# Kernel tuning notes

Measured on AMD Instinct MI355X. Metric: run time of the kernel, lower is better.

The kernel has to match this reference:

```python
import jax, jax.numpy as jnp
import numpy as np

HIDDEN = 256
HORIZON = 24
FMET = 16
OUT = 1
EPS = 1e-5


def setup_inputs() -> dict:
    key = jax.random.key(0)
    ks = jax.random.split(key, 12)
    B, N = 16, 1000
    final_h = jax.random.normal(ks[0], (B, N, HIDDEN), dtype=jnp.float32)
    future_met = jax.random.normal(ks[1], (B, HORIZON, N, FMET), dtype=jnp.float32)
    # step_queries: xavier_uniform over (max_horizon, hidden)
    lim_q = float(np.sqrt(6.0 / (HORIZON + HIDDEN)))
    step_queries = jax.random.uniform(ks[2], (HORIZON, HIDDEN), minval=-lim_q, maxval=lim_q, dtype=jnp.float32)
    # future_met_proj: Linear(FMET -> HIDDEN); store weight as (FMET, HIDDEN)
    lim_fm = float(np.sqrt(1.0 / FMET))
    W_fm = jax.random.uniform(ks[3], (FMET, HIDDEN), minval=-lim_fm, maxval=lim_fm, dtype=jnp.float32)
    b_fm = jax.random.uniform(ks[4], (HIDDEN,), minval=-lim_fm, maxval=lim_fm, dtype=jnp.float32)
    gamma = jnp.ones((HIDDEN,), dtype=jnp.float32)
    beta = jnp.zeros((HIDDEN,), dtype=jnp.float32)
    lim1 = float(np.sqrt(1.0 / HIDDEN))
    W1 = jax.random.uniform(ks[5], (HIDDEN, HIDDEN), minval=-lim1, maxval=lim1, dtype=jnp.float32)
    b1 = jax.random.uniform(ks[6], (HIDDEN,), minval=-lim1, maxval=lim1, dtype=jnp.float32)
    W2 = jax.random.uniform(ks[7], (HIDDEN, OUT), minval=-lim1, maxval=lim1, dtype=jnp.float32)
    b2 = jax.random.uniform(ks[8], (OUT,), minval=-lim1, maxval=lim1, dtype=jnp.float32)
    return {
        "final_h": final_h,
        "future_met": future_met,
        "step_queries": step_queries,
        "W_fm": W_fm,
        "b_fm": b_fm,
        "gamma": gamma,
        "beta": beta,
        "W1": W1,
        "b1": b1,
        "W2": W2,
        "b2": b2,
    }


def _layer_norm(x, gamma, beta):
    mu = jnp.mean(x, axis=-1, keepdims=True)
    var = jnp.mean(jnp.square(x - mu), axis=-1, keepdims=True)
    return (x - mu) * jax.lax.rsqrt(var + EPS) * gamma + beta


def reference(final_h, future_met, step_queries, W_fm, b_fm, gamma, beta, W1, b1, W2, b2):
    # final_h: (B, N, H); future_met: (B, T, N, F)
    # combined: (B, N, T, H) = broadcast(final_h) + queries + proj(future_met)
    combined = final_h[:, :, None, :] + step_queries[None, None, :, :]
    fm = jnp.transpose(future_met, (0, 2, 1, 3))  # (B, N, T, F)
    combined = combined + (jnp.einsum("bntf,fh->bnth", fm, W_fm) + b_fm)
    x = _layer_norm(combined, gamma, beta)
    x = jax.nn.gelu(x @ W1 + b1, approximate=False)
    # dropout is identity in eval mode
    out = x @ W2 + b2  # (B, N, T, OUT)
    return jnp.transpose(out, (0, 2, 1, 3))  # (B, T, N, OUT)
```

## Files before the change

kernel.cpp:

```cpp
#include <hip/hip_runtime.h>
#include <hip/hip_bf16.h>
#include <stdint.h>

#define MROWS 32
#define LDA   264
#define FMS   40

typedef __bf16 bf16x8 __attribute__((ext_vector_type(8)));
typedef float  f32x4  __attribute__((ext_vector_type(4)));

__device__ __forceinline__ unsigned short f2bf(float f) {
    union { float f; uint32_t u; } v; v.f = f;
    return (unsigned short)((v.u + 0x7FFFu + ((v.u >> 16) & 1u)) >> 16);
}

__device__ __forceinline__ ushort2 pk_bf16(float a, float b) {
    union { __hip_bfloat162 v; ushort2 u; } c;
    c.v = __float22bfloat162_rn(make_float2(a, b));
    return c.u;
}

__device__ __forceinline__ float gelu_fast(float v) {
    const float t = v * v;
    const float p = fmaf(0.044715f, t, 1.0f);
    const float u = v * p;
    const float e = __builtin_amdgcn_exp2f(u * -2.3021131160186336f);
    return v * __builtin_amdgcn_rcpf(1.0f + e);
}

__global__ __launch_bounds__(256) void prep1(const float* __restrict__ W1,
                                             const float* __restrict__ step_q,
                                             const float* __restrict__ b_fm,
                                             const float* __restrict__ W_fm,
                                             const float* __restrict__ gamma,
                                             const float* __restrict__ beta,
                                             unsigned short* __restrict__ w1frag,
                                             float* __restrict__ sqb,
                                             unsigned short* __restrict__ wfmfrag,
                                             float* __restrict__ gpart,
                                             float* __restrict__ bpart) {
    const int blk = blockIdx.x, tid = threadIdx.x;
    if (blk < 8) {
        __shared__ unsigned short T[256][40];
        const int kk = blk;
        float sg = 0.f, sb = 0.f;
        #pragma unroll
        for (int r = 0; r < 32; ++r) {
            const int k = (kk << 5) + r;
            const float wv = W1[k * 256 + tid];
            sg = fmaf(gamma[k], wv, sg);
            sb = fmaf(beta[k],  wv, sb);
            T[tid][r] = f2bf(wv);
        }
        gpart[(kk << 8) + tid] = sg;
        bpart[(kk << 8) + tid] = sb;
        __syncthreads();
        #pragma unroll
        for (int f = 0; f < 4; ++f) {
            const int fi = (f << 8) + tid;
            const int l = fi & 63, j = (fi >> 6) & 3, w = fi >> 8;
            const int n = (w << 6) + (j << 4) + (l & 15);
            const uint4 v = *(const uint4*)&T[n][(l >> 4) << 3];
            *(uint4*)&w1frag[((w << 5) + (j << 3) + kk) * 512 + (l << 3)] = v;
        }
    } else if (blk < 32) {
        const int t = blk - 8;
        sqb[t * 256 + tid] = step_q[t * 256 + tid] + b_fm[tid];
    } else {
        const int f  = blk - 32;
        const int fr = (f << 8) + tid;
        const int l = fr & 63, j = (fr >> 6) & 3, w = fr >> 8;
        const int n = (w << 6) + (j << 4) + (l & 15);
        const int qr = l >> 4;
        #pragma unroll
        for (int e = 0; e < 8; ++e) {
            const int k = (qr << 3) + e;
            wfmfrag[(fr << 3) + e] = (k < 16) ? f2bf(W_fm[(k << 8) + n]) : (unsigned short)0;
        }
    }
}

__global__ __launch_bounds__(256) void prep2(const float* __restrict__ gpart,
                                             const float* __restrict__ bpart,
                                             const float* __restrict__ b1,
                                             float* __restrict__ gw1,
                                             float* __restrict__ b1t) {
    const int tid = threadIdx.x;
    float sg = 0.f, sb = 0.f;
    #pragma unroll
    for (int kk = 0; kk < 8; ++kk) {
        sg += gpart[(kk << 8) + tid];
        sb += bpart[(kk << 8) + tid];
    }
    gw1[tid] = sg;
    b1t[tid] = sb + b1[tid];
}

__global__ __launch_bounds__(256, 6) void fused_head(
    const float* __restrict__ final_h, const float* __restrict__ future_met,
    const float* __restrict__ gamma,   const float* __restrict__ W2,
    const float* __restrict__ b2,      const unsigned short* __restrict__ w1frag,
    const float* __restrict__ sqb,     const unsigned short* __restrict__ wfmfrag,
    const float* __restrict__ gw1,     const float* __restrict__ b1t,
    float* __restrict__ out)
{
    __shared__ __align__(16) unsigned short Abuf[MROWS * LDA];
    __shared__ __align__(16) unsigned short fmA[MROWS * FMS];
    __shared__ float2 red[4][MROWS];
    __shared__ float2 mv[MROWS];
    __shared__ float  part[4][MROWS];

    const int tid = threadIdx.x;
    const int w   = tid >> 6;
    const int l   = tid & 63;
    const int col = l & 15;
    const int qr  = l >> 4;
    const int m0  = blockIdx.x * MROWS;
    const int bn0 = m0 / 24;
    const int tt0 = m0 - bn0 * 24;

    if (tid < 128) {
        const int row = tid >> 2, f0 = (tid & 3) << 2;
        const int tta = tt0 + row;
        const int sub = (tta >= 24) + (tta >= 48);
        const int tt  = tta - sub * 24;
        const int bn  = bn0 + sub;
        const int b   = bn / 1000, n = bn - b * 1000;
        const float4 v = *(const float4*)&future_met[((((b * 24 + tt) * 1000) + n) << 4) + f0];
        ushort2 lo = pk_bf16(v.x, v.y), hi = pk_bf16(v.z, v.w);
        ushort4 o; o.x = lo.x; o.y = lo.y; o.z = hi.x; o.w = hi.y;
        *(ushort4*)&fmA[row * FMS + f0] = o;
    }
    {
        const int row = tid >> 3, k = 16 + ((tid & 7) << 1);
        *(unsigned int*)&fmA[row * FMS + k] = 0u;
    }
    __syncthreads();

    float g_[4];
    #pragma unroll
    for (int j = 0; j < 4; ++j) g_[j] = gamma[(w << 6) + (j << 4) + col];

    f32x4 acc[2][4];
    #pragma unroll
    for (int i = 0; i < 2; ++i) {
        #pragma unroll
        for (int r = 0; r < 4; ++r) {
            const int d   = (i << 4) + (qr << 2) + r;
            const int tta = tt0 + d;
            const int sub = (tta >= 24) + (tta >= 48);
            const int tt  = tta - sub * 24;
            const int bn  = bn0 + sub;
            const float* fh = final_h + (bn << 8) + (w << 6) + col;
            const float* sb = sqb + (tt << 8) + (w << 6) + col;
            #pragma unroll
            for (int j = 0; j < 4; ++j)
                acc[i][j][r] = fh[j << 4] + sb[j << 4];
        }
    }
    {
        const bf16x8 af0 = *(const bf16x8*)&fmA[col * FMS + (qr << 3)];
        const bf16x8 af1 = *(const bf16x8*)&fmA[(16 + col) * FMS + (qr << 3)];
        const unsigned short* Bwf = wfmfrag + (w << 11) + (l << 3);
        #pragma unroll
        for (int j = 0; j < 4; ++j) {
            const bf16x8 bf = *(const bf16x8*)(Bwf + (j << 9));
            acc[0][j] = __builtin_amdgcn_mfma_f32_16x16x32_bf16(af0, bf, acc[0][j], 0, 0, 0);
            acc[1][j] = __builtin_amdgcn_mfma_f32_16x16x32_bf16(af1, bf, acc[1][j], 0, 0, 0);
        }
    }

    #pragma unroll
    for (int i = 0; i < 2; ++i) {
        #pragma unroll
        for (int r = 0; r < 4; ++r) {
            const int m = (i << 4) + (qr << 2) + r;
            float s = 0.f, q = 0.f, vj[4];
            #pragma unroll
            for (int j = 0; j < 4; ++j) {
                const float v = acc[i][j][r];
                s += v; q = fmaf(v, v, q);
                vj[j] = v * g_[j];
            }
            s += __shfl_xor(s, 1); q += __shfl_xor(q, 1);
            s += __shfl_xor(s, 2); q += __shfl_xor(q, 2);
            s += __shfl_xor(s, 4); q += __shfl_xor(q, 4);
            s += __shfl_xor(s, 8); q += __shfl_xor(q, 8);
            if (col == 0) red[w][m] = make_float2(s, q);
            const ushort2 p01 = pk_bf16(vj[0], vj[1]);
            const ushort2 p23 = pk_bf16(vj[2], vj[3]);
            unsigned short* Ab = &Abuf[m * LDA + (w << 6) + col];
            Ab[0]  = p01.x; Ab[16] = p01.y;
            Ab[32] = p23.x; Ab[48] = p23.y;
        }
    }
    __syncthreads();

    if (tid < MROWS) {
        const float2 a0 = red[0][tid], a1 = red[1][tid], a2 = red[2][tid], a3 = red[3][tid];
        const float S = a0.x + a1.x + a2.x + a3.x;
        const float Q = a0.y + a1.y + a2.y + a3.y;
        const float mu = S * 0.00390625f;
        const float rstd = rsqrtf(Q * 0.00390625f - mu * mu + 1e-5f);
        mv[tid] = make_float2(mu, rstd);
    }

    #pragma unroll
    for (int i = 0; i < 2; ++i)
        #pragma unroll
        for (int j = 0; j < 4; ++j)
            acc[i][j] = (f32x4){0.f, 0.f, 0.f, 0.f};

    {
        const unsigned short* Bw  = w1frag + (w << 14) + (l << 3);
        const unsigned short* Ab0 = &Abuf[col * LDA + (qr << 3)];
        const unsigned short* Ab1 = &Abuf[(16 + col) * LDA + (qr << 3)];
        #pragma unroll
        for (int kk = 0; kk < 8; ++kk) {
            const bf16x8 a0 = *(const bf16x8*)(Ab0 + (kk << 5));
            const bf16x8 a1 = *(const bf16x8*)(Ab1 + (kk << 5));
            #pragma unroll
            for (int j = 0; j < 4; ++j) {
                const bf16x8 bf = *(const bf16x8*)(Bw + (j << 12) + (kk << 9));
                acc[0][j] = __builtin_amdgcn_mfma_f32_16x16x32_bf16(a0, bf, acc[0][j], 0, 0, 0);
                acc[1][j] = __builtin_amdgcn_mfma_f32_16x16x32_bf16(a1, bf, acc[1][j], 0, 0, 0);
            }
        }
    }

    float gwv[4], btv[4], w2v[4];
    #pragma unroll
    for (int j = 0; j < 4; ++j) {
        const int n = (w << 6) + (j << 4) + col;
        gwv[j] = gw1[n]; btv[j] = b1t[n]; w2v[j] = W2[n];
    }
    __syncthreads();

    #pragma unroll
    for (int i = 0; i < 2; ++i) {
        #pragma unroll
        for (int r = 0; r < 4; ++r) {
            const int m = (i << 4) + (qr << 2) + r;
            const float2 p = mv[m];
            const float cm = -p.x * p.y;
            float pp = 0.f;
            #pragma unroll
            for (int j = 0; j < 4; ++j) {
                const float yv = fmaf(p.y, acc[i][j][r], fmaf(cm, gwv[j], btv[j]));
                const float g = gelu_fast(yv);
                pp = fmaf(g, w2v[j], pp);
            }
            pp += __shfl_xor(pp, 1);
            pp += __shfl_xor(pp, 2);
            pp += __shfl_xor(pp, 4);
            pp += __shfl_xor(pp, 8);
            if (col == 0) part[w][m] = pp;
        }
    }
    __syncthreads();

    if (tid < MROWS) {
        const int m = m0 + tid;
        const float val = part[0][tid] + part[1][tid] + part[2][tid] + part[3][tid] + b2[0];
        const int bn = m / 24, tt = m - bn * 24;
        const int b  = bn / 1000, n = bn - b * 1000;
        out[(b * 24 + tt) * 1000 + n] = val;
    }
}

extern "C" void kernel_launch(void* const* d_in, const int* in_sizes, int n_in,
                              void* d_out, int out_size, void* d_ws, size_t ws_size,
                              hipStream_t stream) {
    const float* final_h    = (const float*)d_in[0];
    const float* future_met = (const float*)d_in[1];
    const float* step_q     = (const float*)d_in[2];
    const float* W_fm       = (const float*)d_in[3];
    const float* b_fm       = (const float*)d_in[4];
    const float* gamma      = (const float*)d_in[5];
    const float* beta       = (const float*)d_in[6];
    const float* W1         = (const float*)d_in[7];
    const float* b1         = (const float*)d_in[8];
    const float* W2         = (const float*)d_in[9];
    const float* b2         = (const float*)d_in[10];

    unsigned short* w1frag  = (unsigned short*)d_ws;
    float*          sqb     = (float*)((char*)d_ws + 131072);
    unsigned short* wfmfrag = (unsigned short*)((char*)d_ws + 155648);
    float*          gw1     = (float*)((char*)d_ws + 188416);
    float*          b1t     = (float*)((char*)d_ws + 189440);
    float*          gpart   = (float*)((char*)d_ws + 190464);
    float*          bpart   = (float*)((char*)d_ws + 198656);
    float* out = (float*)d_out;

    prep1<<<36, 256, 0, stream>>>(W1, step_q, b_fm, W_fm, gamma, beta,
                                  w1frag, sqb, wfmfrag, gpart, bpart);
    prep2<<<1, 256, 0, stream>>>(gpart, bpart, b1, gw1, b1t);
    fused_head<<<12000, 256, 0, stream>>>(final_h, future_met, gamma, W2, b2,
                                          w1frag, sqb, wfmfrag, gw1, b1t, out);
}
```

Baseline: 219.3 us.

## Process two full nodes (48 rows) per block and fold prep2 into main kernel

Each block now handles 48 rows, exactly two (b,n) nodes of 24 horizon steps, instead of 32. This aligns tiles to node boundaries, removes the div/mod index math, and amortizes each W1 fragment load over three MFMA row tiles instead of two. The separate prep2 launch is removed: every block sums the gpart/bpart partials itself, which saves one kernel launch but adds redundant global reads per block. Launch bounds drop from 6 to 5 waves to make room for the larger accumulators and LDS.

```diff
diff --git a/kernel.cpp b/kernel.cpp
--- a/kernel.cpp
+++ b/kernel.cpp
@@ -2,7 +2,7 @@
 #include <hip/hip_bf16.h>
 #include <stdint.h>
 
-#define MROWS 32
+#define MROWS 48
 #define LDA   264
 #define FMS   40
 
@@ -80,29 +80,13 @@
     }
 }
 
-__global__ __launch_bounds__(256) void prep2(const float* __restrict__ gpart,
-                                             const float* __restrict__ bpart,
-                                             const float* __restrict__ b1,
-                                             float* __restrict__ gw1,
-                                             float* __restrict__ b1t) {
-    const int tid = threadIdx.x;
-    float sg = 0.f, sb = 0.f;
-    #pragma unroll
-    for (int kk = 0; kk < 8; ++kk) {
-        sg += gpart[(kk << 8) + tid];
-        sb += bpart[(kk << 8) + tid];
-    }
-    gw1[tid] = sg;
-    b1t[tid] = sb + b1[tid];
-}
-
-__global__ __launch_bounds__(256, 6) void fused_head(
+__global__ __launch_bounds__(256, 5) void fused_head(
     const float* __restrict__ final_h, const float* __restrict__ future_met,
     const float* __restrict__ gamma,   const float* __restrict__ W2,
     const float* __restrict__ b2,      const unsigned short* __restrict__ w1frag,
     const float* __restrict__ sqb,     const unsigned short* __restrict__ wfmfrag,
-    const float* __restrict__ gw1,     const float* __restrict__ b1t,
-    float* __restrict__ out)
+    const float* __restrict__ gpart,   const float* __restrict__ bpart,
+    const float* __restrict__ b1,      float* __restrict__ out)
 {
     __shared__ __align__(16) unsigned short Abuf[MROWS * LDA];
     __shared__ __align__(16) unsigned short fmA[MROWS * FMS];
@@ -116,24 +100,23 @@
     const int col = l & 15;
     const int qr  = l >> 4;
     const int m0  = blockIdx.x * MROWS;
-    const int bn0 = m0 / 24;
-    const int tt0 = m0 - bn0 * 24;
-
-    if (tid < 128) {
+    const int bn0 = blockIdx.x << 1;
+
+    if (tid < 192) {
         const int row = tid >> 2, f0 = (tid & 3) << 2;
-        const int tta = tt0 + row;
-        const int sub = (tta >= 24) + (tta >= 48);
-        const int tt  = tta - sub * 24;
-        const int bn  = bn0 + sub;
+        const int ge  = row >= 24;
+        const int tt  = row - (ge ? 24 : 0);
+        const int bn  = bn0 + ge;
         const int b   = bn / 1000, n = bn - b * 1000;
         const float4 v = *(const float4*)&future_met[((((b * 24 + tt) * 1000) + n) << 4) + f0];
         ushort2 lo = pk_bf16(v.x, v.y), hi = pk_bf16(v.z, v.w);
         ushort4 o; o.x = lo.x; o.y = lo.y; o.z = hi.x; o.w = hi.y;
         *(ushort4*)&fmA[row * FMS + f0] = o;
     }
-    {
-        const int row = tid >> 3, k = 16 + ((tid & 7) << 1);
-        *(unsigned int*)&fmA[row * FMS + k] = 0u;
+    if (tid < 96) {
+        const int row = tid >> 1;
+        const uint4 z = {0u, 0u, 0u, 0u};
+        *(uint4*)&fmA[row * FMS + 16 + ((tid & 1) << 3)] = z;
     }
     __syncthreads();
 
@@ -141,16 +124,15 @@
     #pragma unroll
     for (int j = 0; j < 4; ++j) g_[j] = gamma[(w << 6) + (j << 4) + col];
 
-    f32x4 acc[2][4];
-    #pragma unroll
-    for (int i = 0; i < 2; ++i) {
+    f32x4 acc[3][4];
+    #pragma unroll
+    for (int i = 0; i < 3; ++i) {
         #pragma unroll
         for (int r = 0; r < 4; ++r) {
-            const int d   = (i << 4) + (qr << 2) + r;
-            const int tta = tt0 + d;
-            const int sub = (tta >= 24) + (tta >= 48);
-            const int tt  = tta - sub * 24;
-            const int bn  = bn0 + sub;
+            const int m  = (i << 4) + (qr << 2) + r;
+            const int ge = m >= 24;
+            const int tt = m - (ge ? 24 : 0);
+            const int bn = bn0 + ge;
             const float* fh = final_h + (bn << 8) + (w << 6) + col;
             const float* sb = sqb + (tt << 8) + (w << 6) + col;
             #pragma unroll
@@ -159,19 +141,22 @@
         }
     }
     {
-        const bf16x8 af0 = *(const bf16x8*)&fmA[col * FMS + (qr << 3)];
-        const bf16x8 af1 = *(const bf16x8*)&fmA[(16 + col) * FMS + (qr << 3)];
+        bf16x8 af[3];
+        #pragma unroll
+        for (int i = 0; i < 3; ++i)
+            af[i] = *(const bf16x8*)&fmA[((i << 4) + col) * FMS + (qr << 3)];
         const unsigned short* Bwf = wfmfrag + (w << 11) + (l << 3);
         #pragma unroll
         for (int j = 0; j < 4; ++j) {
             const bf16x8 bf = *(const bf16x8*)(Bwf + (j << 9));
-            acc[0][j] = __builtin_amdgcn_mfma_f32_16x16x32_bf16(af0, bf, acc[0][j], 0, 0, 0);
-            acc[1][j] = __builtin_amdgcn_mfma_f32_16x16x32_bf16(af1, bf, acc[1][j], 0, 0, 0);
-        }
-    }
-
-    #pragma unroll
-    for (int i = 0; i < 2; ++i) {
+            #pragma unroll
+            for (int i = 0; i < 3; ++i)
+                acc[i][j] = __builtin_amdgcn_mfma_f32_16x16x32_bf16(af[i], bf, acc[i][j], 0, 0, 0);
+        }
+    }
+
+    #pragma unroll
+    for (int i = 0; i < 3; ++i) {
         #pragma unroll
         for (int r = 0; r < 4; ++r) {
             const int m = (i << 4) + (qr << 2) + r;
@@ -206,24 +191,27 @@
     }
 
     #pragma unroll
-    for (int i = 0; i < 2; ++i)
+    for (int i = 0; i < 3; ++i)
         #pragma unroll
         for (int j = 0; j < 4; ++j)
             acc[i][j] = (f32x4){0.f, 0.f, 0.f, 0.f};
 
     {
-        const unsigned short* Bw  = w1frag + (w << 14) + (l << 3);
+        const unsigned short* Bw = w1frag + (w << 14) + (l << 3);
         const unsigned short* Ab0 = &Abuf[col * LDA + (qr << 3)];
         const unsigned short* Ab1 = &Abuf[(16 + col) * LDA + (qr << 3)];
+        const unsigned short* Ab2 = &Abuf[(32 + col) * LDA + (qr << 3)];
         #pragma unroll
         for (int kk = 0; kk < 8; ++kk) {
             const bf16x8 a0 = *(const bf16x8*)(Ab0 + (kk << 5));
             const bf16x8 a1 = *(const bf16x8*)(Ab1 + (kk << 5));
+            const bf16x8 a2 = *(const bf16x8*)(Ab2 + (kk << 5));
             #pragma unroll
             for (int j = 0; j < 4; ++j) {
                 const bf16x8 bf = *(const bf16x8*)(Bw + (j << 12) + (kk << 9));
                 acc[0][j] = __builtin_amdgcn_mfma_f32_16x16x32_bf16(a0, bf, acc[0][j], 0, 0, 0);
                 acc[1][j] = __builtin_amdgcn_mfma_f32_16x16x32_bf16(a1, bf, acc[1][j], 0, 0, 0);
+                acc[2][j] = __builtin_amdgcn_mfma_f32_16x16x32_bf16(a2, bf, acc[2][j], 0, 0, 0);
             }
         }
     }
@@ -232,12 +220,18 @@
     #pragma unroll
     for (int j = 0; j < 4; ++j) {
         const int n = (w << 6) + (j << 4) + col;
-        gwv[j] = gw1[n]; btv[j] = b1t[n]; w2v[j] = W2[n];
-    }
-    __syncthreads();
-
-    #pragma unroll
-    for (int i = 0; i < 2; ++i) {
+        float sg = 0.f, sb = 0.f;
+        #pragma unroll
+        for (int kk = 0; kk < 8; ++kk) {
+            sg += gpart[(kk << 8) + n];
+            sb += bpart[(kk << 8) + n];
+        }
+        gwv[j] = sg; btv[j] = sb + b1[n]; w2v[j] = W2[n];
+    }
+    __syncthreads();
+
+    #pragma unroll
+    for (int i = 0; i < 3; ++i) {
         #pragma unroll
         for (int r = 0; r < 4; ++r) {
             const int m = (i << 4) + (qr << 2) + r;
@@ -260,9 +254,10 @@
     __syncthreads();
 
     if (tid < MROWS) {
-        const int m = m0 + tid;
         const float val = part[0][tid] + part[1][tid] + part[2][tid] + part[3][tid] + b2[0];
-        const int bn = m / 24, tt = m - bn * 24;
+        const int ge = tid >= 24;
+        const int tt = tid - (ge ? 24 : 0);
+        const int bn = bn0 + ge;
         const int b  = bn / 1000, n = bn - b * 1000;
         out[(b * 24 + tt) * 1000 + n] = val;
     }
@@ -286,15 +281,12 @@
     unsigned short* w1frag  = (unsigned short*)d_ws;
     float*          sqb     = (float*)((char*)d_ws + 131072);
     unsigned short* wfmfrag = (unsigned short*)((char*)d_ws + 155648);
-    float*          gw1     = (float*)((char*)d_ws + 188416);
-    float*          b1t     = (float*)((char*)d_ws + 189440);
-    float*          gpart   = (float*)((char*)d_ws + 190464);
-    float*          bpart   = (float*)((char*)d_ws + 198656);
+    float*          gpart   = (float*)((char*)d_ws + 188416);
+    float*          bpart   = (float*)((char*)d_ws + 196608);
     float* out = (float*)d_out;
 
     prep1<<<36, 256, 0, stream>>>(W1, step_q, b_fm, W_fm, gamma, beta,
                                   w1frag, sqb, wfmfrag, gpart, bpart);
-    prep2<<<1, 256, 0, stream>>>(gpart, bpart, b1, gw1, b1t);
-    fused_head<<<12000, 256, 0, stream>>>(final_h, future_met, gamma, W2, b2,
-                                          w1frag, sqb, wfmfrag, gw1, b1t, out);
-}
+    fused_head<<<8000, 256, 0, stream>>>(final_h, future_met, gamma, W2, b2,
+                                         w1frag, sqb, wfmfrag, gpart, bpart, b1, out);
+}
```

Result: slower. 274.2 us (+25.0%).
